# Performance work log

Measured on AMD Instinct MI355X. Metric: run time of the kernel, lower is better.

Reference implementation:

```python
import jax, jax.numpy as jnp
import numpy as np

N_NEIGHBOR = 32


def setup_inputs() -> dict:
    key = jax.random.key(0)
    k1, k2, k3 = jax.random.split(key, 3)
    B, N, S, C = 4, 8192, 2048, 64
    xyz = jax.random.normal(k1, (B, N, 3), dtype=jnp.float32)
    new_xyz = jax.random.normal(k2, (B, S, 3), dtype=jnp.float32)
    features = jax.random.normal(k3, (B, N, C), dtype=jnp.float32)
    return {"xyz": xyz, "new_xyz": new_xyz, "features": features}


def reference(xyz, new_xyz, features):
    # L2 distance map: [B, S, N]
    diff = new_xyz[:, :, None, :3] - xyz[:, None, :, :3]
    dist_map = jnp.sqrt(jnp.sum(diff * diff, axis=-1))
    # full sort then slice top-k (matches torch.sort + [..., :k])
    idx_sorted = jnp.argsort(dist_map, axis=-1)          # [B, S, N]
    similar_idxs = idx_sorted[..., :N_NEIGHBOR]          # [B, S, k]
    similar_value = jnp.take_along_axis(dist_map, similar_idxs, axis=-1)  # [B, S, k]
    # gather neighbor xyz / features: [B, S, k, 3], [B, S, k, C]
    neighbor_xyz = jnp.take_along_axis(xyz[:, None, :, :], similar_idxs[..., None], axis=2)
    neighbor_feature = jnp.take_along_axis(features[:, None, :, :], similar_idxs[..., None], axis=2)
    return neighbor_xyz, similar_idxs, neighbor_feature, similar_value
```

## Files before the change

kernel.cpp:

```cpp
#include <hip/hip_runtime.h>

#define THREADS 256
#define QPB 2
#define KNN 32
#define CAP 512
#define NBIN 256
#define BINBASE 0x790

constexpr int Bc = 4, Nc = 8192, Sc = 2048, Cch = 64;

__global__ __launch_bounds__(THREADS) void neighbor_group_kernel(
    const float* __restrict__ xyz,
    const float* __restrict__ new_xyz,
    const float* __restrict__ feat,
    float* __restrict__ out)
{
  __shared__ unsigned hist[QPB][NBIN];
  __shared__ unsigned candDb[QPB][CAP];
  __shared__ unsigned candIdx[QPB][CAP];
  __shared__ unsigned winIdx[QPB][KNN];
  __shared__ unsigned winDb[QPB][KNN];
  __shared__ unsigned ccnt[QPB];
  __shared__ unsigned sEdge[QPB];
  __shared__ unsigned wsum[4];

  const int tid = threadIdx.x;
  const int q0 = blockIdx.x * QPB;
  const int b = q0 >> 11;

  ((unsigned*)hist)[tid] = 0u;
  ((unsigned*)hist)[tid + THREADS] = 0u;
  if (tid < QPB) ccnt[tid] = 0u;
  __syncthreads();

  float qx[QPB], qy[QPB], qz[QPB];
#pragma unroll
  for (int qi = 0; qi < QPB; ++qi) {
    qx[qi] = new_xyz[(q0 + qi) * 3 + 0];
    qy[qi] = new_xyz[(q0 + qi) * 3 + 1];
    qz[qi] = new_xyz[(q0 + qi) * 3 + 2];
  }

  const float4* __restrict__ xb4 = (const float4*)(xyz + (size_t)b * Nc * 3);

  unsigned keys[QPB][32];

#pragma unroll
  for (int j2 = 0; j2 < 8; ++j2) {
    const int g = tid + j2 * THREADS;
    const float4 f0 = xb4[3 * g + 0];
    const float4 f1 = xb4[3 * g + 1];
    const float4 f2 = xb4[3 * g + 2];
    const float px[4] = {f0.x, f0.w, f1.z, f2.y};
    const float py[4] = {f0.y, f1.x, f1.w, f2.z};
    const float pz[4] = {f0.z, f1.y, f2.x, f2.w};
#pragma unroll
    for (int k = 0; k < 4; ++k) {
#pragma unroll
      for (int qi = 0; qi < QPB; ++qi) {
        const float dx = __fsub_rn(qx[qi], px[k]);
        const float dy = __fsub_rn(qy[qi], py[k]);
        const float dz = __fsub_rn(qz[qi], pz[k]);
        const float s2 = __fadd_rn(
            __fadd_rn(__fmul_rn(dx, dx), __fmul_rn(dy, dy)),
            __fmul_rn(dz, dz));
        const unsigned kb = __float_as_uint(s2);
        keys[qi][j2 * 4 + k] = kb;
        const int bin = min(255, max(0, (int)(kb >> 19) - BINBASE));
        atomicAdd(&hist[qi][bin], 1u);
      }
    }
  }
  __syncthreads();

#pragma unroll
  for (int qi = 0; qi < QPB; ++qi) {
    const unsigned h = hist[qi][tid];
    unsigned v = h;
#pragma unroll
    for (int m = 1; m < 64; m <<= 1) {
      const unsigned u = (unsigned)__shfl_up((int)v, m, 64);
      if ((tid & 63) >= m) v += u;
    }
    if ((tid & 63) == 63) wsum[tid >> 6] = v;
    __syncthreads();
    unsigned off = 0;
    for (int w = 0; w < (tid >> 6); ++w) off += wsum[w];
    const unsigned cum = v + off;
    if (cum >= KNN && (cum - h) < KNN) {
      sEdge[qi] = (unsigned)(BINBASE + tid + 1) << 19;
    }
    __syncthreads();
  }

#pragma unroll
  for (int qi = 0; qi < QPB; ++qi) {
    const unsigned edge = sEdge[qi];
#pragma unroll
    for (int j = 0; j < 32; ++j) {
      if (keys[qi][j] < edge) {
        const unsigned pos = atomicAdd(&ccnt[qi], 1u);
        if (pos < CAP) {
          candDb[qi][pos] = keys[qi][j];
          candIdx[qi][pos] = (unsigned)(4 * tid + (j >> 2) * 1024 + (j & 3));
        }
      }
    }
  }
  __syncthreads();

#pragma unroll
  for (int qi = 0; qi < QPB; ++qi) {
    const unsigned Cc = min(ccnt[qi], (unsigned)CAP);
    for (unsigned t = tid; t < Cc; t += THREADS)
      candDb[qi][t] =
          __float_as_uint(__fsqrt_rn(__uint_as_float(candDb[qi][t])));
  }
  __syncthreads();

#pragma unroll
  for (int qi = 0; qi < QPB; ++qi) {
    const unsigned Cc = min(ccnt[qi], (unsigned)CAP);
    for (unsigned t = tid; t < Cc; t += THREADS) {
      const unsigned mdb = candDb[qi][t];
      const unsigned mix = candIdx[qi][t];
      unsigned rank = 0;
      for (unsigned o = 0; o < Cc; ++o) {
        const unsigned odb = candDb[qi][o];
        const unsigned oix = candIdx[qi][o];
        rank += (odb < mdb || (odb == mdb && oix < mix)) ? 1u : 0u;
      }
      if (rank < KNN) { winIdx[qi][rank] = mix; winDb[qi][rank] = mdb; }
    }
  }
  __syncthreads();

  float* out_nx = out;
  float* out_id = out + (size_t)Bc * Sc * KNN * 3;
  float* out_nf = out_id + (size_t)Bc * Sc * KNN;
  float* out_sv = out_nf + (size_t)Bc * Sc * KNN * Cch;

  const float* xb = xyz + (size_t)b * Nc * 3;
  const float4* fb4 = (const float4*)(feat + (size_t)b * Nc * Cch);

#pragma unroll
  for (int qi = 0; qi < QPB; ++qi) {
    const int q = q0 + qi;
    if (tid < KNN) {
      out_id[(size_t)q * KNN + tid] = (float)winIdx[qi][tid];
      out_sv[(size_t)q * KNN + tid] = __uint_as_float(winDb[qi][tid]);
    }
    if (tid < KNN * 3) {
      const int w = tid / 3, c3 = tid % 3;
      out_nx[((size_t)q * KNN + w) * 3 + c3] =
          xb[(size_t)winIdx[qi][w] * 3 + c3];
    }
    float4* onf4 = (float4*)(out_nf + (size_t)q * KNN * Cch);
#pragma unroll
    for (int r = 0; r < 2; ++r) {
      const int flat = tid + r * THREADS;
      const int w = flat >> 4;
      const int c4 = flat & 15;
      onf4[w * 16 + c4] = fb4[(size_t)winIdx[qi][w] * 16 + c4];
    }
  }
}

extern "C" void kernel_launch(void* const* d_in, const int* in_sizes, int n_in,
                              void* d_out, int out_size, void* d_ws, size_t ws_size,
                              hipStream_t stream) {
  const float* xyz     = (const float*)d_in[0];
  const float* new_xyz = (const float*)d_in[1];
  const float* feat    = (const float*)d_in[2];
  float* out = (float*)d_out;

  const int grid = (Bc * Sc) / QPB;
  neighbor_group_kernel<<<grid, THREADS, 0, stream>>>(xyz, new_xyz, feat, out);
}
```

Before: 68.05 us.

## Replace fixed histogram threshold with per-wave ballot pivot and recompute pass

Drops the shared-memory histogram with hard-coded bin base and the 64-register key cache. A first pass now keeps only a per-thread minimum squared distance. A 31-step ballot bisection per wave then finds the 8th-smallest thread minimum, and the max over the four waves serves as the candidate threshold. A second pass recomputes distances from global xyz and compacts candidates below the pivot, with a bisection retry loop if the count falls outside [32, 512]. This removes histogram atomics and register pressure, which may raise occupancy, at the cost of reading xyz twice and possibly extra retry passes.

```diff
diff --git a/kernel.cpp b/kernel.cpp
--- a/kernel.cpp
+++ b/kernel.cpp
@@ -4,10 +4,18 @@
 #define QPB 2
 #define KNN 32
 #define CAP 512
-#define NBIN 256
-#define BINBASE 0x790
+#define MAXRETRY 34
 
 constexpr int Bc = 4, Nc = 8192, Sc = 2048, Cch = 64;
+
+__device__ __forceinline__ unsigned dist2bits(float qx, float qy, float qz,
+                                              float x, float y, float z) {
+  const float dx = __fsub_rn(qx, x);
+  const float dy = __fsub_rn(qy, y);
+  const float dz = __fsub_rn(qz, z);
+  return __float_as_uint(__fadd_rn(
+      __fadd_rn(__fmul_rn(dx, dx), __fmul_rn(dy, dy)), __fmul_rn(dz, dz)));
+}
 
 __global__ __launch_bounds__(THREADS) void neighbor_group_kernel(
     const float* __restrict__ xyz,
@@ -15,36 +23,29 @@
     const float* __restrict__ feat,
     float* __restrict__ out)
 {
-  __shared__ unsigned hist[QPB][NBIN];
   __shared__ unsigned candDb[QPB][CAP];
   __shared__ unsigned candIdx[QPB][CAP];
   __shared__ unsigned winIdx[QPB][KNN];
   __shared__ unsigned winDb[QPB][KNN];
   __shared__ unsigned ccnt[QPB];
-  __shared__ unsigned sEdge[QPB];
-  __shared__ unsigned wsum[4];
+  __shared__ unsigned wavePiv[QPB][4];
 
-  const int tid = threadIdx.x;
-  const int q0 = blockIdx.x * QPB;
-  const int b = q0 >> 11;
+  const int tid  = threadIdx.x;
+  const int lane = tid & 63;
+  const int wid  = tid >> 6;
+  const int q0   = blockIdx.x * QPB;
+  const int b    = q0 >> 11;
 
-  ((unsigned*)hist)[tid] = 0u;
-  ((unsigned*)hist)[tid + THREADS] = 0u;
-  if (tid < QPB) ccnt[tid] = 0u;
-  __syncthreads();
-
-  float qx[QPB], qy[QPB], qz[QPB];
-#pragma unroll
-  for (int qi = 0; qi < QPB; ++qi) {
-    qx[qi] = new_xyz[(q0 + qi) * 3 + 0];
-    qy[qi] = new_xyz[(q0 + qi) * 3 + 1];
-    qz[qi] = new_xyz[(q0 + qi) * 3 + 2];
-  }
+  const float qx0 = new_xyz[q0 * 3 + 0];
+  const float qy0 = new_xyz[q0 * 3 + 1];
+  const float qz0 = new_xyz[q0 * 3 + 2];
+  const float qx1 = new_xyz[q0 * 3 + 3];
+  const float qy1 = new_xyz[q0 * 3 + 4];
+  const float qz1 = new_xyz[q0 * 3 + 5];
 
   const float4* __restrict__ xb4 = (const float4*)(xyz + (size_t)b * Nc * 3);
 
-  unsigned keys[QPB][32];
-
+  unsigned lmin0 = 0xFFFFFFFFu, lmin1 = 0xFFFFFFFFu;
 #pragma unroll
   for (int j2 = 0; j2 < 8; ++j2) {
     const int g = tid + j2 * THREADS;
@@ -56,71 +57,89 @@
     const float pz[4] = {f0.z, f1.y, f2.x, f2.w};
 #pragma unroll
     for (int k = 0; k < 4; ++k) {
+      const unsigned k0 = dist2bits(qx0, qy0, qz0, px[k], py[k], pz[k]);
+      const unsigned k1 = dist2bits(qx1, qy1, qz1, px[k], py[k], pz[k]);
+      lmin0 = min(lmin0, k0);
+      lmin1 = min(lmin1, k1);
+    }
+  }
+
+  unsigned P0 = 0u, P1 = 0u;
 #pragma unroll
-      for (int qi = 0; qi < QPB; ++qi) {
-        const float dx = __fsub_rn(qx[qi], px[k]);
-        const float dy = __fsub_rn(qy[qi], py[k]);
-        const float dz = __fsub_rn(qz[qi], pz[k]);
-        const float s2 = __fadd_rn(
-            __fadd_rn(__fmul_rn(dx, dx), __fmul_rn(dy, dy)),
-            __fmul_rn(dz, dz));
-        const unsigned kb = __float_as_uint(s2);
-        keys[qi][j2 * 4 + k] = kb;
-        const int bin = min(255, max(0, (int)(kb >> 19) - BINBASE));
-        atomicAdd(&hist[qi][bin], 1u);
+  for (int bb = 30; bb >= 0; --bb) {
+    const unsigned t0 = P0 | (1u << bb);
+    const unsigned t1 = P1 | (1u << bb);
+    const unsigned long long m0 = __ballot(lmin0 < t0);
+    const unsigned long long m1 = __ballot(lmin1 < t1);
+    if (__popcll(m0) < 8) P0 = t0;
+    if (__popcll(m1) < 8) P1 = t1;
+  }
+  if (lane == 0) { wavePiv[0][wid] = P0 + 1u; wavePiv[1][wid] = P1 + 1u; }
+  __syncthreads();
+  unsigned piv0 = max(max(wavePiv[0][0], wavePiv[0][1]),
+                      max(wavePiv[0][2], wavePiv[0][3]));
+  unsigned piv1 = max(max(wavePiv[1][0], wavePiv[1][1]),
+                      max(wavePiv[1][2], wavePiv[1][3]));
+
+  unsigned lo0 = 0u, hi0 = 0xFFFFFFFFu, lo1 = 0u, hi1 = 0xFFFFFFFFu;
+  bool forced0 = false, forced1 = false;
+  unsigned C0 = 0, C1 = 0;
+  for (int it = 0; it < MAXRETRY; ++it) {
+    __syncthreads();
+    if (tid < QPB) ccnt[tid] = 0u;
+    __syncthreads();
+#pragma unroll
+    for (int j2 = 0; j2 < 8; ++j2) {
+      const int g = tid + j2 * THREADS;
+      const float4 f0 = xb4[3 * g + 0];
+      const float4 f1 = xb4[3 * g + 1];
+      const float4 f2 = xb4[3 * g + 2];
+      const float px[4] = {f0.x, f0.w, f1.z, f2.y};
+      const float py[4] = {f0.y, f1.x, f1.w, f2.z};
+      const float pz[4] = {f0.z, f1.y, f2.x, f2.w};
+#pragma unroll
+      for (int k = 0; k < 4; ++k) {
+        const unsigned pidx = (unsigned)(4 * g + k);
+        const unsigned k0 = dist2bits(qx0, qy0, qz0, px[k], py[k], pz[k]);
+        if (k0 < piv0) {
+          const unsigned pos = atomicAdd(&ccnt[0], 1u);
+          if (pos < CAP) { candDb[0][pos] = k0; candIdx[0][pos] = pidx; }
+        }
+        const unsigned k1 = dist2bits(qx1, qy1, qz1, px[k], py[k], pz[k]);
+        if (k1 < piv1) {
+          const unsigned pos = atomicAdd(&ccnt[1], 1u);
+          if (pos < CAP) { candDb[1][pos] = k1; candIdx[1][pos] = pidx; }
+        }
       }
     }
+    __syncthreads();
+    const unsigned c0 = ccnt[0], c1 = ccnt[1];
+    C0 = min(c0, (unsigned)CAP);
+    C1 = min(c1, (unsigned)CAP);
+    const bool ok0 = forced0 || (c0 >= KNN && c0 <= CAP);
+    const bool ok1 = forced1 || (c1 >= KNN && c1 <= CAP);
+    if (ok0 && ok1) break;
+    if (!ok0) {
+      if (c0 < KNN) lo0 = piv0; else hi0 = piv0;
+      if (hi0 - lo0 <= 1u) { piv0 = hi0; forced0 = true; }
+      else piv0 = lo0 + ((hi0 - lo0) >> 1);
+    }
+    if (!ok1) {
+      if (c1 < KNN) lo1 = piv1; else hi1 = piv1;
+      if (hi1 - lo1 <= 1u) { piv1 = hi1; forced1 = true; }
+      else piv1 = lo1 + ((hi1 - lo1) >> 1);
+    }
   }
+
+  for (unsigned t = tid; t < C0; t += THREADS)
+    candDb[0][t] = __float_as_uint(__fsqrt_rn(__uint_as_float(candDb[0][t])));
+  for (unsigned t = tid; t < C1; t += THREADS)
+    candDb[1][t] = __float_as_uint(__fsqrt_rn(__uint_as_float(candDb[1][t])));
   __syncthreads();
 
 #pragma unroll
   for (int qi = 0; qi < QPB; ++qi) {
-    const unsigned h = hist[qi][tid];
-    unsigned v = h;
-#pragma unroll
-    for (int m = 1; m < 64; m <<= 1) {
-      const unsigned u = (unsigned)__shfl_up((int)v, m, 64);
-      if ((tid & 63) >= m) v += u;
-    }
-    if ((tid & 63) == 63) wsum[tid >> 6] = v;
-    __syncthreads();
-    unsigned off = 0;
-    for (int w = 0; w < (tid >> 6); ++w) off += wsum[w];
-    const unsigned cum = v + off;
-    if (cum >= KNN && (cum - h) < KNN) {
-      sEdge[qi] = (unsigned)(BINBASE + tid + 1) << 19;
-    }
-    __syncthreads();
-  }
-
-#pragma unroll
-  for (int qi = 0; qi < QPB; ++qi) {
-    const unsigned edge = sEdge[qi];
-#pragma unroll
-    for (int j = 0; j < 32; ++j) {
-      if (keys[qi][j] < edge) {
-        const unsigned pos = atomicAdd(&ccnt[qi], 1u);
-        if (pos < CAP) {
-          candDb[qi][pos] = keys[qi][j];
-          candIdx[qi][pos] = (unsigned)(4 * tid + (j >> 2) * 1024 + (j & 3));
-        }
-      }
-    }
-  }
-  __syncthreads();
-
-#pragma unroll
-  for (int qi = 0; qi < QPB; ++qi) {
-    const unsigned Cc = min(ccnt[qi], (unsigned)CAP);
-    for (unsigned t = tid; t < Cc; t += THREADS)
-      candDb[qi][t] =
-          __float_as_uint(__fsqrt_rn(__uint_as_float(candDb[qi][t])));
-  }
-  __syncthreads();
-
-#pragma unroll
-  for (int qi = 0; qi < QPB; ++qi) {
-    const unsigned Cc = min(ccnt[qi], (unsigned)CAP);
+    const unsigned Cc = (qi == 0) ? C0 : C1;
     for (unsigned t = tid; t < Cc; t += THREADS) {
       const unsigned mdb = candDb[qi][t];
       const unsigned mix = candIdx[qi][t];
```

After: 113.0 us. +66.1%, slower.

## Replace histogram threshold with ballot pivot search and recompute-based candidate collection

Applied to the files above, without the earlier changes.

Drops the per-query shared-memory histogram with atomics and the register-held key array. Each query now takes a per-thread minimum distance, and a ballot bit search over those minima picks a pivot that guarantees at least 32 points fall below it. The kernel then rescans all points, recomputing distances and collecting candidates under the pivot, and binary-searches the pivot if the count falls outside [32, CAP]. Queries per block rise from 2 to 8 so each xyz load is shared by more queries, and the rank sort is spread one wave per query. The cost is recomputing distances on every rescan and possible extra retry passes when the pivot is too loose.

```diff
diff --git a/kernel.cpp b/kernel.cpp
--- a/kernel.cpp
+++ b/kernel.cpp
@@ -1,13 +1,22 @@
 #include <hip/hip_runtime.h>
 
 #define THREADS 256
-#define QPB 2
+#define QPB 8
 #define KNN 32
 #define CAP 512
-#define NBIN 256
-#define BINBASE 0x790
+#define MAXRETRY 34
+#define NOTDONE 0xFFFFFFFFu
 
 constexpr int Bc = 4, Nc = 8192, Sc = 2048, Cch = 64;
+
+__device__ __forceinline__ unsigned dist2bits(float qx, float qy, float qz,
+                                              float x, float y, float z) {
+  const float dx = __fsub_rn(qx, x);
+  const float dy = __fsub_rn(qy, y);
+  const float dz = __fsub_rn(qz, z);
+  return __float_as_uint(__fadd_rn(
+      __fadd_rn(__fmul_rn(dx, dx), __fmul_rn(dy, dy)), __fmul_rn(dz, dz)));
+}
 
 __global__ __launch_bounds__(THREADS) void neighbor_group_kernel(
     const float* __restrict__ xyz,
@@ -15,23 +24,20 @@
     const float* __restrict__ feat,
     float* __restrict__ out)
 {
-  __shared__ unsigned hist[QPB][NBIN];
   __shared__ unsigned candDb[QPB][CAP];
   __shared__ unsigned candIdx[QPB][CAP];
   __shared__ unsigned winIdx[QPB][KNN];
   __shared__ unsigned winDb[QPB][KNN];
   __shared__ unsigned ccnt[QPB];
-  __shared__ unsigned sEdge[QPB];
-  __shared__ unsigned wsum[4];
-
-  const int tid = threadIdx.x;
-  const int q0 = blockIdx.x * QPB;
-  const int b = q0 >> 11;
-
-  ((unsigned*)hist)[tid] = 0u;
-  ((unsigned*)hist)[tid + THREADS] = 0u;
-  if (tid < QPB) ccnt[tid] = 0u;
-  __syncthreads();
+  __shared__ unsigned wavePiv[4][QPB];
+  __shared__ unsigned sPiv[QPB], sLo[QPB], sHi[QPB], sForce[QPB], sC[QPB];
+  __shared__ unsigned sDone;
+
+  const int tid  = threadIdx.x;
+  const int lane = tid & 63;
+  const int wid  = tid >> 6;
+  const int q0   = blockIdx.x * QPB;
+  const int b    = q0 >> 11;
 
   float qx[QPB], qy[QPB], qz[QPB];
 #pragma unroll
@@ -43,8 +49,9 @@
 
   const float4* __restrict__ xb4 = (const float4*)(xyz + (size_t)b * Nc * 3);
 
-  unsigned keys[QPB][32];
-
+  unsigned lmin[QPB];
+#pragma unroll
+  for (int qi = 0; qi < QPB; ++qi) lmin[qi] = NOTDONE;
 #pragma unroll
   for (int j2 = 0; j2 < 8; ++j2) {
     const int g = tid + j2 * THREADS;
@@ -58,60 +65,85 @@
     for (int k = 0; k < 4; ++k) {
 #pragma unroll
       for (int qi = 0; qi < QPB; ++qi) {
-        const float dx = __fsub_rn(qx[qi], px[k]);
-        const float dy = __fsub_rn(qy[qi], py[k]);
-        const float dz = __fsub_rn(qz[qi], pz[k]);
-        const float s2 = __fadd_rn(
-            __fadd_rn(__fmul_rn(dx, dx), __fmul_rn(dy, dy)),
-            __fmul_rn(dz, dz));
-        const unsigned kb = __float_as_uint(s2);
-        keys[qi][j2 * 4 + k] = kb;
-        const int bin = min(255, max(0, (int)(kb >> 19) - BINBASE));
-        atomicAdd(&hist[qi][bin], 1u);
-      }
-    }
+        const unsigned kb = dist2bits(qx[qi], qy[qi], qz[qi], px[k], py[k], pz[k]);
+        lmin[qi] = min(lmin[qi], kb);
+      }
+    }
+  }
+
+#pragma unroll
+  for (int qi = 0; qi < QPB; ++qi) {
+    unsigned P = 0u;
+#pragma unroll
+    for (int bb = 30; bb >= 0; --bb) {
+      const unsigned t = P | (1u << bb);
+      if (__popcll(__ballot(lmin[qi] < t)) < 8) P = t;
+    }
+    if (lane == 0) wavePiv[wid][qi] = P + 1u;
   }
   __syncthreads();
 
-#pragma unroll
-  for (int qi = 0; qi < QPB; ++qi) {
-    const unsigned h = hist[qi][tid];
-    unsigned v = h;
-#pragma unroll
-    for (int m = 1; m < 64; m <<= 1) {
-      const unsigned u = (unsigned)__shfl_up((int)v, m, 64);
-      if ((tid & 63) >= m) v += u;
-    }
-    if ((tid & 63) == 63) wsum[tid >> 6] = v;
-    __syncthreads();
-    unsigned off = 0;
-    for (int w = 0; w < (tid >> 6); ++w) off += wsum[w];
-    const unsigned cum = v + off;
-    if (cum >= KNN && (cum - h) < KNN) {
-      sEdge[qi] = (unsigned)(BINBASE + tid + 1) << 19;
-    }
-    __syncthreads();
-  }
-
-#pragma unroll
-  for (int qi = 0; qi < QPB; ++qi) {
-    const unsigned edge = sEdge[qi];
-#pragma unroll
-    for (int j = 0; j < 32; ++j) {
-      if (keys[qi][j] < edge) {
-        const unsigned pos = atomicAdd(&ccnt[qi], 1u);
-        if (pos < CAP) {
-          candDb[qi][pos] = keys[qi][j];
-          candIdx[qi][pos] = (unsigned)(4 * tid + (j >> 2) * 1024 + (j & 3));
+  if (tid < QPB) {
+    const unsigned p = max(max(wavePiv[0][tid], wavePiv[1][tid]),
+                           max(wavePiv[2][tid], wavePiv[3][tid]));
+    sPiv[tid] = p;
+    sLo[tid] = 0u; sHi[tid] = 0xFFFFFFFFu; sForce[tid] = 0u;
+    sC[tid] = NOTDONE;
+  }
+
+  for (int it = 0; it < MAXRETRY; ++it) {
+    __syncthreads();
+    if (tid < QPB && sC[tid] == NOTDONE) ccnt[tid] = 0u;
+    if (tid == 0) sDone = 1u;
+    __syncthreads();
+
+    unsigned piv[QPB];
+#pragma unroll
+    for (int qi = 0; qi < QPB; ++qi)
+      piv[qi] = (sC[qi] == NOTDONE) ? sPiv[qi] : 0u;
+
+#pragma unroll
+    for (int j2 = 0; j2 < 8; ++j2) {
+      const int g = tid + j2 * THREADS;
+      const float4 f0 = xb4[3 * g + 0];
+      const float4 f1 = xb4[3 * g + 1];
+      const float4 f2 = xb4[3 * g + 2];
+      const float px[4] = {f0.x, f0.w, f1.z, f2.y};
+      const float py[4] = {f0.y, f1.x, f1.w, f2.z};
+      const float pz[4] = {f0.z, f1.y, f2.x, f2.w};
+#pragma unroll
+      for (int k = 0; k < 4; ++k) {
+        const unsigned pidx = (unsigned)(4 * g + k);
+#pragma unroll
+        for (int qi = 0; qi < QPB; ++qi) {
+          const unsigned kb = dist2bits(qx[qi], qy[qi], qz[qi], px[k], py[k], pz[k]);
+          if (kb < piv[qi]) {
+            const unsigned pos = atomicAdd(&ccnt[qi], 1u);
+            if (pos < CAP) { candDb[qi][pos] = kb; candIdx[qi][pos] = pidx; }
+          }
         }
       }
     }
-  }
-  __syncthreads();
-
-#pragma unroll
-  for (int qi = 0; qi < QPB; ++qi) {
-    const unsigned Cc = min(ccnt[qi], (unsigned)CAP);
+    __syncthreads();
+
+    if (tid < QPB && sC[tid] == NOTDONE) {
+      const unsigned c = ccnt[tid];
+      if (sForce[tid] || (c >= KNN && c <= CAP)) {
+        sC[tid] = min(c, (unsigned)CAP);
+      } else {
+        if (c < KNN) sLo[tid] = sPiv[tid]; else sHi[tid] = sPiv[tid];
+        if (sHi[tid] - sLo[tid] <= 1u) { sPiv[tid] = sHi[tid]; sForce[tid] = 1u; }
+        else sPiv[tid] = sLo[tid] + ((sHi[tid] - sLo[tid]) >> 1);
+        sDone = 0u;
+      }
+    }
+    __syncthreads();
+    if (sDone) break;
+  }
+
+#pragma unroll
+  for (int qi = 0; qi < QPB; ++qi) {
+    const unsigned Cc = sC[qi];
     for (unsigned t = tid; t < Cc; t += THREADS)
       candDb[qi][t] =
           __float_as_uint(__fsqrt_rn(__uint_as_float(candDb[qi][t])));
@@ -119,12 +151,13 @@
   __syncthreads();
 
 #pragma unroll
-  for (int qi = 0; qi < QPB; ++qi) {
-    const unsigned Cc = min(ccnt[qi], (unsigned)CAP);
-    for (unsigned t = tid; t < Cc; t += THREADS) {
+  for (int rr = 0; rr < 2; ++rr) {
+    const int qi = wid + rr * 4;
+    const unsigned Cc = sC[qi];
+    for (unsigned t = lane; t < Cc; t += 64) {
       const unsigned mdb = candDb[qi][t];
       const unsigned mix = candIdx[qi][t];
-      unsigned rank = 0;
+      unsigned rank = 0u;
       for (unsigned o = 0; o < Cc; ++o) {
         const unsigned odb = candDb[qi][o];
         const unsigned oix = candIdx[qi][o];
```

Result: slower. 250.9 us (+268.7%).
